# Optimization experiments

Measured on AMD Instinct MI355X. Metric: run time of the kernel, lower is better.

Reference implementation:

```python
import jax, jax.numpy as jnp
import numpy as np

B, S, H, I, E = 4, 2048, 768, 3072, 8
TOP_K = 2
ALPHA_BALANCE = 0.01
ENERGY_ALPHA = 0.0


def setup_inputs() -> dict:
    key = jax.random.key(0)
    ks = jax.random.split(key, 5)
    g = lambda k, shape: jax.random.normal(k, shape, jnp.float32) * 0.02
    return {
        "hidden_states": jax.random.normal(ks[0], (B, S, H), jnp.float32),
        "router_w": g(ks[1], (H, E)),
        "router_b": jnp.zeros((E,), jnp.float32),
        "w1": g(ks[2], (E, H, I)),
        "b1": jnp.zeros((E, I), jnp.float32),
        "w2": g(ks[3], (E, I, H)),
        "b2": jnp.zeros((E, H), jnp.float32),
    }


def reference(hidden_states, router_w, router_b, w1, b1, w2, b2):
    # --- routing: top-2 softmax gate scattered back to dense [B,S,E] ---
    router_logits = hidden_states @ router_w + router_b          # [B,S,E]
    top_v, top_i = jax.lax.top_k(router_logits, TOP_K)           # [B,S,2]
    top_w = jax.nn.softmax(top_v, axis=-1)                       # [B,S,2]
    gating = jnp.sum(
        jax.nn.one_hot(top_i, E, dtype=router_logits.dtype) * top_w[..., None],
        axis=-2,
    )                                                            # [B,S,E]

    # --- aux losses (torch .std() is unbiased, ddof=1) ---
    importance = gating.sum(axis=(0, 1))                         # [E]
    mean_imp = importance.mean()
    load_balancing_loss = ALPHA_BALANCE * (
        jnp.var(importance, ddof=1) / (mean_imp ** 2 + 1e-8)
    )
    probs_mean = gating.mean(axis=(0, 1))                        # [E]
    energy_loss = ENERGY_ALPHA * jnp.sum(probs_mean ** 2)
    aux_loss = load_balancing_loss + energy_loss

    # --- dense all-expert FFN (faithful to the naive original) ---
    # h: [B,S,E,I]; exact (erf) GELU matches torch nn.GELU default
    h = jax.nn.gelu(
        jnp.einsum("bsh,ehf->bsef", hidden_states, w1) + b1,
        approximate=False,
    )
    expert_outputs = jnp.einsum("bsef,efh->bseh", h, w2) + b2    # [B,S,E,H]
    # dropout is identity in eval mode

    # --- weighted combine (the bmm in the original) ---
    final_output = jnp.einsum("bse,bseh->bsh", gating, expert_outputs)
    return final_output, aux_loss, gating
```

## Files before the change

### kernel.cpp

```cpp
#include <hip/hip_runtime.h>
#include <math.h>

#define NB 4
#define NS 2048
#define HD 768
#define ID 3072
#define NE 8
#define NTOK (NB*NS)
#define NPAIR (NTOK*2)

#define BMF 128
#define BN1 128
#define BNF 256
#define BKF 64
#define MAXTF 136

#define BMS 32
#define KCH 128
#define NCHUNK (ID/KCH)
#define MAXTS (NPAIR/BMS + NE)
#define LDP 36

typedef unsigned short u16;
typedef __attribute__((ext_vector_type(8))) short bf16x8;
typedef __attribute__((ext_vector_type(4))) float f32x4;

__device__ __forceinline__ float bf2f(u16 u) {
  union { unsigned int i; float f; } v; v.i = ((unsigned int)u) << 16; return v.f;
}
__device__ __forceinline__ u16 f2bf(float f) {
  union { float fl; unsigned int i; } v; v.fl = f;
  unsigned int r = v.i + 0x7fffu + ((v.i >> 16) & 1u);
  return (u16)(r >> 16);
}
__device__ __forceinline__ void gload16(const void* g, void* l) {
  __builtin_amdgcn_global_load_lds(
      (const __attribute__((address_space(1))) void*)g,
      (__attribute__((address_space(3))) void*)l, 16, 0, 0);
}
__device__ __forceinline__ float gelu_fast(float x) {
  float u = 0.7978845608028654f * (x + 0.044715f * x * x * x);
  float e = __expf(2.f * u);
  float t = 1.f - 2.f / (e + 1.f);
  return 0.5f * x * (1.f + t);
}
__device__ __forceinline__ int xcd_swz_2d() {
  int nwg  = gridDim.x * gridDim.y;
  int orig = blockIdx.x + blockIdx.y * gridDim.x;
  int q = nwg >> 3, r = nwg & 7;
  int xcd = orig & 7, i = orig >> 3;
  return (xcd < r) ? (xcd * (q + 1) + i) : (r * (q + 1) + (xcd - r) * q + i);
}

__global__ __launch_bounds__(256) void router_kernel(
    const float* __restrict__ x, const float* __restrict__ rw,
    const float* __restrict__ rb, float* __restrict__ gating,
    int* __restrict__ topi, float* __restrict__ topw, u16* __restrict__ xb)
{
  int wid = threadIdx.x >> 6, lane = threadIdx.x & 63;
  int tok = blockIdx.x * 4 + wid;
  float acc[NE];
  #pragma unroll
  for (int e = 0; e < NE; ++e) acc[e] = 0.f;
  const float* xr = x + (size_t)tok * HD;
  float4 xq[3];
  #pragma unroll
  for (int r = 0; r < 3; ++r) {
    int h4 = (r*64 + lane) * 4;
    float4 xv = *(const float4*)&xr[h4];
    xq[r] = xv;
    const float4* wr = (const float4*)(rw + (size_t)h4 * NE);
    float4 a0 = wr[0], c0 = wr[1], a1 = wr[2], c1 = wr[3];
    float4 a2 = wr[4], c2 = wr[5], a3 = wr[6], c3 = wr[7];
    acc[0] += xv.x*a0.x + xv.y*a1.x + xv.z*a2.x + xv.w*a3.x;
    acc[1] += xv.x*a0.y + xv.y*a1.y + xv.z*a2.y + xv.w*a3.y;
    acc[2] += xv.x*a0.z + xv.y*a1.z + xv.z*a2.z + xv.w*a3.z;
    acc[3] += xv.x*a0.w + xv.y*a1.w + xv.z*a2.w + xv.w*a3.w;
    acc[4] += xv.x*c0.x + xv.y*c1.x + xv.z*c2.x + xv.w*c3.x;
    acc[5] += xv.x*c0.y + xv.y*c1.y + xv.z*c2.y + xv.w*c3.y;
    acc[6] += xv.x*c0.z + xv.y*c1.z + xv.z*c2.z + xv.w*c3.z;
    acc[7] += xv.x*c0.w + xv.y*c1.w + xv.z*c2.w + xv.w*c3.w;
  }
  if (xb) {
    u16* xo = xb + (size_t)tok * HD;
    #pragma unroll
    for (int r = 0; r < 3; ++r) {
      int h4 = (r*64 + lane) * 4;
      ushort4 o;
      o.x = f2bf(xq[r].x); o.y = f2bf(xq[r].y);
      o.z = f2bf(xq[r].z); o.w = f2bf(xq[r].w);
      *(ushort4*)&xo[h4] = o;
    }
  }
  #pragma unroll
  for (int off = 1; off < 64; off <<= 1) {
    #pragma unroll
    for (int e = 0; e < NE; ++e) acc[e] += __shfl_xor(acc[e], off);
  }
  float lg[NE];
  #pragma unroll
  for (int e = 0; e < NE; ++e) lg[e] = acc[e] + rb[e];
  int i0 = 0;
  #pragma unroll
  for (int e = 1; e < NE; ++e) if (lg[e] > lg[i0]) i0 = e;
  int i1 = (i0 == 0) ? 1 : 0;
  #pragma unroll
  for (int e = 0; e < NE; ++e) if (e != i0 && lg[e] > lg[i1]) i1 = e;
  float ex = expf(lg[i1] - lg[i0]);
  float s = 1.f + ex;
  float w0 = 1.f / s, w1v = ex / s;
  if (lane < NE)
    gating[(size_t)tok*NE + lane] = (lane==i0) ? w0 : (lane==i1 ? w1v : 0.f);
  if (lane == 0) {
    topi[2*tok] = i0; topi[2*tok+1] = i1;
    topw[2*tok] = w0; topw[2*tok+1] = w1v;
  }
}

__global__ __launch_bounds__(1024) void plan_kernel(
    const int* __restrict__ topi, const float* __restrict__ topw,
    int* __restrict__ offs, int* __restrict__ tilesc,
    int* __restrict__ ptok, float* __restrict__ pwv, int bm,
    float* __restrict__ aux)
{
  __shared__ int   wcnt[16][NE];
  __shared__ int   wbase[16][NE];
  __shared__ float wsum[16][NE];
  int tid = threadIdx.x, w = tid >> 6, lane = tid & 63;
  int base = w * 1024;

  int cnt[NE];
  #pragma unroll
  for (int e = 0; e < NE; ++e) cnt[e] = 0;
  #pragma unroll
  for (int it = 0; it < 16; ++it) {
    int ti = topi[base + it*64 + lane];
    #pragma unroll
    for (int e = 0; e < NE; ++e) {
      unsigned long long m = __ballot(ti == e);
      cnt[e] += __popcll(m);
    }
  }
  if (lane == 0)
    #pragma unroll
    for (int e = 0; e < NE; ++e) wcnt[w][e] = cnt[e];
  __syncthreads();

  if (tid == 0) {
    int o = 0, tt = 0;
    for (int e = 0; e < NE; ++e) {
      offs[e] = o; tilesc[e] = tt;
      int run = o, tot = 0;
      for (int ww = 0; ww < 16; ++ww) { wbase[ww][e] = run; run += wcnt[ww][e]; tot += wcnt[ww][e]; }
      o += tot;
      tt += (tot + bm - 1) / bm;
    }
    offs[NE] = o; tilesc[NE] = tt;
  }
  __syncthreads();

  int run[NE];
  float lsum[NE];
  #pragma unroll
  for (int e = 0; e < NE; ++e) { run[e] = wbase[w][e]; lsum[e] = 0.f; }
  unsigned long long lt = (1ull << lane) - 1ull;
  #pragma unroll
  for (int it = 0; it < 16; ++it) {
    int p = base + it*64 + lane;
    int ti = topi[p];
    float tw = topw[p];
    int idx = 0;
    #pragma unroll
    for (int e = 0; e < NE; ++e) {
      unsigned long long m = __ballot(ti == e);
      int r = run[e] + __popcll(m & lt);
      if (ti == e) idx = r;
      run[e] += __popcll(m);
      lsum[e] += (ti == e) ? tw : 0.f;
    }
    ptok[idx] = p >> 1;
    pwv[idx] = tw;
  }
  #pragma unroll
  for (int off = 1; off < 64; off <<= 1) {
    #pragma unroll
    for (int e = 0; e < NE; ++e) lsum[e] += __shfl_xor(lsum[e], off);
  }
  if (lane == 0)
    #pragma unroll
    for (int e = 0; e < NE; ++e) wsum[w][e] = lsum[e];
  __syncthreads();
  if (tid == 0) {
    float imp[NE];
    for (int e = 0; e < NE; ++e) {
      float s = 0.f;
      for (int ww = 0; ww < 16; ++ww) s += wsum[ww][e];
      imp[e] = s;
    }
    float mean = 0.f;
    for (int e = 0; e < NE; ++e) mean += imp[e];
    mean *= (1.f/NE);
    float var = 0.f;
    for (int e = 0; e < NE; ++e) { float d = imp[e] - mean; var += d*d; }
    var *= (1.f/(NE-1));
    aux[0] = 0.01f * var / (mean*mean + 1e-8f);
  }
}

__global__ __launch_bounds__(256) void transpose_bf16_kernel(
    const float* __restrict__ src, u16* __restrict__ dst, int R, int C)
{
  __shared__ u16 tile[64][65];
  int e = blockIdx.z;
  const float* s = src + (size_t)e * R * C;
  u16* d = dst + (size_t)e * R * C;
  int c0 = blockIdx.x * 64, r0 = blockIdx.y * 64;
  int t = threadIdx.x;
  int rr = t >> 4, c4 = (t & 15) * 4;
  #pragma unroll
  for (int rep = 0; rep < 4; ++rep) {
    int r = rr + rep * 16;
    float4 v = *(const float4*)&s[(size_t)(r0 + r) * C + c0 + c4];
    tile[r][c4+0] = f2bf(v.x); tile[r][c4+1] = f2bf(v.y);
    tile[r][c4+2] = f2bf(v.z); tile[r][c4+3] = f2bf(v.w);
  }
  __syncthreads();
  #pragma unroll
  for (int rep = 0; rep < 4; ++rep) {
    int w = t + rep * 256;
    int c = w >> 4, rq = (w & 15) * 4;
    ushort4 o;
    o.x = tile[rq+0][c]; o.y = tile[rq+1][c];
    o.z = tile[rq+2][c]; o.w = tile[rq+3][c];
    *(ushort4*)&d[(size_t)(c0 + c) * R + r0 + rq] = o;
  }
}

__global__ __launch_bounds__(256, 3) void moe_gemm1_kernel(
    const u16* __restrict__ xbf, const u16* __restrict__ w1t,
    const float* __restrict__ b1, const int* __restrict__ offs,
    const int* __restrict__ tilesc, const int* __restrict__ ptok,
    const float* __restrict__ pwv, u16* __restrict__ hbuf, int t0)
{
  __shared__ __align__(16) u16 As[BMF*BKF];
  __shared__ __align__(16) u16 Bs[BN1*BKF];
  __shared__ int   toks_s[BMF];
  __shared__ float gws_s[BMF];

  int wkid = xcd_swz_2d();
  int tile = wkid % gridDim.x;
  int n0   = (wkid / gridDim.x) * BN1;

  int t = t0 + tile;
  if (t >= tilesc[NE]) return;
  int e = 0;
  #pragma unroll
  for (int k = 1; k < NE; ++k) if (t >= tilesc[k]) e = k;
  int row0 = offs[e] + (t - tilesc[e]) * BMF;
  int nrows = offs[e+1] - row0; if (nrows > BMF) nrows = BMF;
  int tid = threadIdx.x, wid = tid >> 6, lane = tid & 63;

  if (tid < BMF) {
    int tk = -1; float g = 0.f;
    if (tid < nrows) { tk = ptok[row0 + tid]; g = pwv[row0 + tid]; }
    toks_s[tid] = tk; gws_s[tid] = g;
  }
  __syncthreads();

  int srow = tid >> 3;
  int swz  = ((tid & 7) << 4) ^ ((srow & 7) << 4);
  const char* aS[4]; const char* bS[4];
  u16* aD[4]; u16* bD[4];
  #pragma unroll
  for (int g = 0; g < 4; ++g) {
    int tk = toks_s[g*32 + srow]; if (tk < 0) tk = 0;
    aS[g] = (const char*)xbf + (size_t)tk * (HD*2) + swz;
    bS[g] = (const char*)w1t + ((size_t)e*ID + n0 + g*32 + srow) * (HD*2) + swz;
    aD[g] = As + g*2048 + wid*512;
    bD[g] = Bs + g*2048 + wid*512;
  }

  int wr = wid >> 1, wc = wid & 1;
  int lr = lane & 15, lg = lane >> 4;

  f32x4 acc[4][4];
  #pragma unroll
  for (int m = 0; m < 4; ++m)
    #pragma unroll
    for (int n = 0; n < 4; ++n) { f32x4 z = {0.f,0.f,0.f,0.f}; acc[m][n] = z; }

  for (int ks = 0; ks < HD/BKF; ++ks) {
    __syncthreads();
    int ko = ks * 128;
    #pragma unroll
    for (int g = 0; g < 4; ++g) gload16(aS[g] + ko, aD[g]);
    #pragma unroll
    for (int g = 0; g < 4; ++g) gload16(bS[g] + ko, bD[g]);
    __syncthreads();
    #pragma unroll
    for (int k2 = 0; k2 < 2; ++k2) {
      bf16x8 af[4], bfr[4];
      #pragma unroll
      for (int m = 0; m < 4; ++m) {
        int row = wr*64 + m*16 + lr;
        int bo = (k2*64 + lg*16) ^ ((row & 7) << 4);
        af[m] = *(const bf16x8*)((const char*)As + row*128 + bo);
      }
      #pragma unroll
      for (int n = 0; n < 4; ++n) {
        int row = wc*64 + n*16 + lr;
        int bo = (k2*64 + lg*16) ^ ((row & 7) << 4);
        bfr[n] = *(const bf16x8*)((const char*)Bs + row*128 + bo);
      }
      #pragma unroll
      for (int m = 0; m < 4; ++m)
        #pragma unroll
        for (int n = 0; n < 4; ++n)
          acc[m][n] = __builtin_amdgcn_mfma_f32_16x16x32_bf16(af[m], bfr[n], acc[m][n], 0, 0, 0);
    }
  }

  int rbase = wr*64, cbase = n0 + wc*64;
  const float* b1e = b1 + (size_t)e * ID;
  float b1v[4];
  #pragma unroll
  for (int n = 0; n < 4; ++n) b1v[n] = b1e[cbase + n*16 + lr];
  size_t hrow0 = (size_t)tile * BMF;
  #pragma unroll
  for (int m = 0; m < 4; ++m) {
    #pragma unroll
    for (int j = 0; j < 4; ++j) {
      int row = rbase + m*16 + lg*4 + j;
      float g = gws_s[row];
      u16* hp = hbuf + (hrow0 + row) * ID + cbase + lr;
      #pragma unroll
      for (int n = 0; n < 4; ++n) {
        float v = acc[m][n][j] + b1v[n];
        hp[n*16] = f2bf(gelu_fast(v) * g);
      }
    }
  }
}

__global__ __launch_bounds__(512, 2) void moe_gemm2_kernel(
    const u16* __restrict__ hbuf, const u16* __restrict__ w2t,
    const float* __restrict__ b2, const int* __restrict__ offs,
    const int* __restrict__ tilesc, const int* __restrict__ ptok,
    const float* __restrict__ pwv, float* __restrict__ out, int t0)
{
  __shared__ __align__(16) u16 As[BMF*BKF];
  __shared__ __align__(16) u16 Bs[BNF*BKF];
  __shared__ int   toks_s[BMF];
  __shared__ float gws_s[BMF];

  int wkid = xcd_swz_2d();
  int tile = wkid % gridDim.x;
  int n0   = (wkid / gridDim.x) * BNF;

  int t = t0 + tile;
  if (t >= tilesc[NE]) return;
  int e = 0;
  #pragma unroll
  for (int k = 1; k < NE; ++k) if (t >= tilesc[k]) e = k;
  int row0 = offs[e] + (t - tilesc[e]) * BMF;
  int nrows = offs[e+1] - row0; if (nrows > BMF) nrows = BMF;
  int tid = threadIdx.x, wid = tid >> 6, lane = tid & 63;

  if (tid < BMF) {
    int tk = -1; float g = 0.f;
    if (tid < nrows) { tk = ptok[row0 + tid]; g = pwv[row0 + tid]; }
    toks_s[tid] = tk; gws_s[tid] = g;
  }
  __syncthreads();

  int ssub = tid >> 3;
  int sbc  = (tid & 7) << 4;
  int swz  = sbc ^ ((ssub & 7) << 4);
  const char* aS0 = (const char*)hbuf + ((size_t)tile*BMF +       ssub) * (ID*2) + swz;
  const char* aS1 = (const char*)hbuf + ((size_t)tile*BMF +  64 + ssub) * (ID*2) + swz;
  const char* bS0 = (const char*)w2t + ((size_t)e*HD + n0 +       ssub) * (ID*2) + swz;
  const char* bS1 = (const char*)w2t + ((size_t)e*HD + n0 +  64 + ssub) * (ID*2) + swz;
  const char* bS2 = (const char*)w2t + ((size_t)e*HD + n0 + 128 + ssub) * (ID*2) + swz;
  const char* bS3 = (const char*)w2t + ((size_t)e*HD + n0 + 192 + ssub) * (ID*2) + swz;
  u16* aD0 = As + wid*512;
  u16* aD1 = As + 4096 + wid*512;
  u16* bD0 = Bs + wid*512;
  u16* bD1 = Bs +  4096 + wid*512;
  u16* bD2 = Bs +  8192 + wid*512;
  u16* bD3 = Bs + 12288 + wid*512;

  int wr = wid >> 2, wc = wid & 3;
  int lr = lane & 15, lg = lane >> 4;

  f32x4 acc[4][4];
  #pragma unroll
  for (int m = 0; m < 4; ++m)
    #pragma unroll
    for (int n = 0; n < 4; ++n) { f32x4 zz = {0.f,0.f,0.f,0.f}; acc[m][n] = zz; }

  for (int ks = 0; ks < ID/BKF; ++ks) {
    __syncthreads();
    int ko = ks * 128;
    gload16(aS0 + ko, aD0);
    gload16(aS1 + ko, aD1);
    gload16(bS0 + ko, bD0);
    gload16(bS1 + ko, bD1);
    gload16(bS2 + ko, bD2);
    gload16(bS3 + ko, bD3);
    __syncthreads();
    #pragma unroll
    for (int k2 = 0; k2 < 2; ++k2) {
      bf16x8 af[4], bfr[4];
      #pragma unroll
      for (int m = 0; m < 4; ++m) {
        int row = wr*64 + m*16 + lr;
        int bo = (k2*64 + lg*16) ^ ((row & 7) << 4);
        af[m] = *(const bf16x8*)((const char*)As + row*128 + bo);
      }
      #pragma unroll
      for (int n = 0; n < 4; ++n) {
        int row = wc*64 + n*16 + lr;
        int bo = (k2*64 + lg*16) ^ ((row & 7) << 4);
        bfr[n] = *(const bf16x8*)((const char*)Bs + row*128 + bo);
      }
      #pragma unroll
      for (int m = 0; m < 4; ++m)
        #pragma unroll
        for (int n = 0; n < 4; ++n)
          acc[m][n] = __builtin_amdgcn_mfma_f32_16x16x32_bf16(af[m], bfr[n], acc[m][n], 0, 0, 0);
    }
  }

  int rbase = wr*64, cbase = n0 + wc*64;
  const float* b2e = b2 + (size_t)e * HD;
  float b2v[4];
  #pragma unroll
  for (int n = 0; n < 4; ++n) b2v[n] = b2e[cbase + n*16 + lr];
  #pragma unroll
  for (int m = 0; m < 4; ++m) {
    #pragma unroll
    for (int j = 0; j < 4; ++j) {
      int row = rbase + m*16 + lg*4 + j;
      int tk = toks_s[row];
      if (tk < 0) continue;
      float g = gws_s[row];
      float* op = out + (size_t)tk * HD + cbase + lr;
      #pragma unroll
      for (int n = 0; n < 4; ++n)
        atomicAdd(&op[n*16], acc[m][n][j] + g * b2v[n]);
    }
  }
}

__global__ __launch_bounds__(512, 4) void ffn_kernel(
    const float* __restrict__ x, const float* __restrict__ w1,
    const float* __restrict__ b1, const float* __restrict__ w2,
    const float* __restrict__ b2, const int* __restrict__ offs,
    const int* __restrict__ tilesc, const int* __restrict__ ptok,
    const float* __restrict__ pwv, float* __restrict__ out)
{
  __shared__ u16 x_t[HD][LDP];
  __shared__ u16 h_t[KCH][LDP];
  __shared__ int   toks[BMS];
  __shared__ float gws[BMS];

  int bid = blockIdx.x;
  if (bid >= tilesc[NE]) return;
  int e = 0;
  #pragma unroll
  for (int k = 1; k < NE; ++k) if (bid >= tilesc[k]) e = k;
  int tile = bid - tilesc[e];
  int row0 = offs[e] + tile * BMS;
  int nrows = offs[e+1] - row0;
  if (nrows > BMS) nrows = BMS;

  int tid = threadIdx.x;
  if (tid < BMS) {
    int tk = -1; float g = 0.f;
    if (tid < nrows) { tk = ptok[row0 + tid]; g = pwv[row0 + tid]; }
    toks[tid] = tk; gws[tid] = g;
  }
  __syncthreads();

  for (int idx = tid; idx < BMS*HD; idx += 512) {
    int m = idx / HD, h = idx - m*HD;
    int tk = toks[m];
    x_t[h][m] = (tk >= 0) ? f2bf(x[(size_t)tk*HD + h]) : (u16)0;
  }

  int w4 = (tid >> 6) << 2;
  int lane = tid & 63;
  const float* w1e = w1 + (size_t)e * HD * ID;
  const float* w2e = w2 + (size_t)e * ID * HD;
  const float* b1e = b1 + (size_t)e * ID;
  const float* b2e = b2 + (size_t)e * HD;

  float acc[4][12];
  #pragma unroll
  for (int jm = 0; jm < 4; ++jm)
    #pragma unroll
    for (int jn = 0; jn < 12; ++jn) acc[jm][jn] = 0.f;

  __syncthreads();
  float gwr[4];
  #pragma unroll
  for (int jm = 0; jm < 4; ++jm) gwr[jm] = gws[w4 + jm];

  for (int c = 0; c < NCHUNK; ++c) {
    int i0 = c * KCH;
    float hb[4][2];
    #pragma unroll
    for (int jm = 0; jm < 4; ++jm) { hb[jm][0] = 0.f; hb[jm][1] = 0.f; }
    const float* p = w1e + i0 + lane;
    #pragma unroll 4
    for (int h = 0; h < HD; ++h) {
      ushort4 xu = *(const ushort4*)&x_t[h][w4];
      float wv0 = p[0];
      float wv1 = p[64];
      p += ID;
      float x0 = bf2f(xu.x), x1 = bf2f(xu.y), x2 = bf2f(xu.z), x3 = bf2f(xu.w);
      hb[0][0] += x0*wv0; hb[1][0] += x1*wv0; hb[2][0] += x2*wv0; hb[3][0] += x3*wv0;
      hb[0][1] += x0*wv1; hb[1][1] += x1*wv1; hb[2][1] += x2*wv1; hb[3][1] += x3*wv1;
    }
    float b1v0 = b1e[i0 + lane];
    float b1v1 = b1e[i0 + 64 + lane];
    __syncthreads();
    #pragma unroll
    for (int q = 0; q < 2; ++q) {
      int il = lane + 64*q;
      float bv = q ? b1v1 : b1v0;
      #pragma unroll
      for (int jm = 0; jm < 4; ++jm) {
        float v = hb[jm][q] + bv;
        v = 0.5f * v * (1.f + erff(v * 0.70710678118654752f));
        h_t[il][w4 + jm] = f2bf(v * gwr[jm]);
      }
    }
    __syncthreads();
    const float* q2 = w2e + (size_t)i0 * HD + lane;
    for (int k = 0; k < KCH; ++k) {
      ushort4 hu = *(const ushort4*)&h_t[k][w4];
      float h0 = bf2f(hu.x), h1 = bf2f(hu.y), h2 = bf2f(hu.z), h3 = bf2f(hu.w);
      #pragma unroll
      for (int jn = 0; jn < 12; ++jn) {
        float wv = q2[64*jn];
        acc[0][jn] += h0*wv; acc[1][jn] += h1*wv;
        acc[2][jn] += h2*wv; acc[3][jn] += h3*wv;
      }
      q2 += HD;
    }
  }

  #pragma unroll
  for (int jm = 0; jm < 4; ++jm) {
    int m = w4 + jm;
    int tk = toks[m];
    if (tk < 0) continue;
    float g = gwr[jm];
    float* orow = out + (size_t)tk * HD;
    #pragma unroll
    for (int jn = 0; jn < 12; ++jn) {
      int n = lane + 64*jn;
      atomicAdd(&orow[n], acc[jm][jn] + g * b2e[n]);
    }
  }
}

extern "C" void kernel_launch(void* const* d_in, const int* in_sizes, int n_in,
                              void* d_out, int out_size, void* d_ws, size_t ws_size,
                              hipStream_t stream)
{
  const float* x  = (const float*)d_in[0];
  const float* rw = (const float*)d_in[1];
  const float* rb = (const float*)d_in[2];
  const float* w1 = (const float*)d_in[3];
  const float* b1 = (const float*)d_in[4];
  const float* w2 = (const float*)d_in[5];
  const float* b2 = (const float*)d_in[6];

  float* out    = (float*)d_out;
  float* aux    = out + (size_t)NTOK * HD;
  float* gating = aux + 1;

  int*   W  = (int*)d_ws;
  float* Wf = (float*)d_ws;
  int*   offs   = W + 16;
  int*   tilesc = W + 32;
  int*   topi   = W + 64;
  float* topw   = Wf + 64 + NPAIR;
  int*   ptok   = W + 64 + 2*NPAIR;
  float* pwv    = Wf + 64 + 3*NPAIR;
  char*  wsB    = (char*)d_ws;
  const size_t OFF_XBF = 262400;
  const size_t OFF_W1T = OFF_XBF + (size_t)NTOK*HD*2;
  const size_t OFF_W2T = OFF_W1T + (size_t)NE*ID*HD*2;
  const size_t OFF_H   = OFF_W2T + (size_t)NE*ID*HD*2;
  const size_t NEED_FULL = OFF_H + (size_t)MAXTF*BMF*ID*2;

  u16* xbf = (u16*)(wsB + OFF_XBF);
  u16* w1t = (u16*)(wsB + OFF_W1T);
  u16* w2t = (u16*)(wsB + OFF_W2T);
  u16* hb  = (u16*)(wsB + OFF_H);

  bool fast = (ws_size >= NEED_FULL);

  hipMemsetAsync(d_out, 0, (size_t)NTOK * HD * sizeof(float), stream);

  router_kernel<<<NTOK/4, 256, 0, stream>>>(x, rw, rb, gating, topi, topw,
                                            fast ? xbf : (u16*)nullptr);

  if (fast) {
    plan_kernel<<<1, 1024, 0, stream>>>(topi, topw, offs, tilesc, ptok, pwv, BMF, aux);
    transpose_bf16_kernel<<<dim3(ID/64, HD/64, NE), 256, 0, stream>>>(w1, w1t, HD, ID);
    transpose_bf16_kernel<<<dim3(HD/64, ID/64, NE), 256, 0, stream>>>(w2, w2t, ID, HD);
    moe_gemm1_kernel<<<dim3(MAXTF, ID/BN1), 256, 0, stream>>>(
        xbf, w1t, b1, offs, tilesc, ptok, pwv, hb, 0);
    moe_gemm2_kernel<<<dim3(MAXTF, HD/BNF), 512, 0, stream>>>(
        hb, w2t, b2, offs, tilesc, ptok, pwv, out, 0);
  } else {
    plan_kernel<<<1, 1024, 0, stream>>>(topi, topw, offs, tilesc, ptok, pwv, BMS, aux);
    ffn_kernel<<<MAXTS, 512, 0, stream>>>(x, w1, b1, w2, b2, offs, tilesc, ptok, pwv, out);
  }
}
```

Baseline: 320.8 us.

## Fuse router and weight transposes into one prep kernel; retile gemm2 to 128x128

Router, w1 transpose and w2 transpose now run as one launch, dispatched by block index, which cuts launch overhead and lets the three jobs overlap. GEMM2 moves from 512-thread blocks with 256-wide N tiles to 256-thread blocks with 128-wide N tiles and occupancy hint 4, giving more blocks for better load balance at the cost of reloading A tiles more often. Both GEMMs switch to a 1D grid with an XCD swizzle that places the N-tiles of one M-tile next to each other, aiming for better L2 reuse of activations.

```diff
diff --git a/kernel.cpp b/kernel.cpp
--- a/kernel.cpp
+++ b/kernel.cpp
@@ -11,9 +11,11 @@
 
 #define BMF 128
 #define BN1 128
-#define BNF 256
+#define BN2 128
 #define BKF 64
 #define MAXTF 136
+#define NY1 (ID/BN1)
+#define NY2 (HD/BN2)
 
 #define BMS 32
 #define KCH 128
@@ -44,21 +46,21 @@
   float t = 1.f - 2.f / (e + 1.f);
   return 0.5f * x * (1.f + t);
 }
-__device__ __forceinline__ int xcd_swz_2d() {
-  int nwg  = gridDim.x * gridDim.y;
-  int orig = blockIdx.x + blockIdx.y * gridDim.x;
+__device__ __forceinline__ int xcd_swz_1d() {
+  int nwg  = gridDim.x;
+  int orig = blockIdx.x;
   int q = nwg >> 3, r = nwg & 7;
   int xcd = orig & 7, i = orig >> 3;
   return (xcd < r) ? (xcd * (q + 1) + i) : (r * (q + 1) + (xcd - r) * q + i);
 }
 
-__global__ __launch_bounds__(256) void router_kernel(
-    const float* __restrict__ x, const float* __restrict__ rw,
+__device__ __forceinline__ void router_body(
+    int bid, const float* __restrict__ x, const float* __restrict__ rw,
     const float* __restrict__ rb, float* __restrict__ gating,
     int* __restrict__ topi, float* __restrict__ topw, u16* __restrict__ xb)
 {
   int wid = threadIdx.x >> 6, lane = threadIdx.x & 63;
-  int tok = blockIdx.x * 4 + wid;
+  int tok = bid * 4 + wid;
   float acc[NE];
   #pragma unroll
   for (int e = 0; e < NE; ++e) acc[e] = 0.f;
@@ -117,6 +119,69 @@
   }
 }
 
+__device__ __forceinline__ void transpose_body(
+    int bx, int by, int e, const float* __restrict__ src, u16* __restrict__ dst,
+    int R, int C)
+{
+  __shared__ u16 tile[64][65];
+  const float* s = src + (size_t)e * R * C;
+  u16* d = dst + (size_t)e * R * C;
+  int c0 = bx * 64, r0 = by * 64;
+  int t = threadIdx.x;
+  int rr = t >> 4, c4 = (t & 15) * 4;
+  #pragma unroll
+  for (int rep = 0; rep < 4; ++rep) {
+    int r = rr + rep * 16;
+    float4 v = *(const float4*)&s[(size_t)(r0 + r) * C + c0 + c4];
+    tile[r][c4+0] = f2bf(v.x); tile[r][c4+1] = f2bf(v.y);
+    tile[r][c4+2] = f2bf(v.z); tile[r][c4+3] = f2bf(v.w);
+  }
+  __syncthreads();
+  #pragma unroll
+  for (int rep = 0; rep < 4; ++rep) {
+    int w = t + rep * 256;
+    int c = w >> 4, rq = (w & 15) * 4;
+    ushort4 o;
+    o.x = tile[rq+0][c]; o.y = tile[rq+1][c];
+    o.z = tile[rq+2][c]; o.w = tile[rq+3][c];
+    *(ushort4*)&d[(size_t)(c0 + c) * R + r0 + rq] = o;
+  }
+}
+
+#define NW1T ((ID/64)*(HD/64)*NE)
+#define NW2T ((HD/64)*(ID/64)*NE)
+__global__ __launch_bounds__(256) void prep_kernel(
+    const float* __restrict__ x, const float* __restrict__ rw,
+    const float* __restrict__ rb, float* __restrict__ gating,
+    int* __restrict__ topi, float* __restrict__ topw, u16* __restrict__ xb,
+    const float* __restrict__ w1, u16* __restrict__ w1t,
+    const float* __restrict__ w2, u16* __restrict__ w2t)
+{
+  int bid = blockIdx.x;
+  if (bid < NTOK/4) { router_body(bid, x, rw, rb, gating, topi, topw, xb); return; }
+  bid -= NTOK/4;
+  if (bid < NW1T) {
+    int bx = bid % (ID/64); int rest = bid / (ID/64);
+    int by = rest % (HD/64); int e = rest / (HD/64);
+    transpose_body(bx, by, e, w1, w1t, HD, ID);
+    return;
+  }
+  bid -= NW1T;
+  {
+    int bx = bid % (HD/64); int rest = bid / (HD/64);
+    int by = rest % (ID/64); int e = rest / (ID/64);
+    transpose_body(bx, by, e, w2, w2t, ID, HD);
+  }
+}
+
+__global__ __launch_bounds__(256) void router_kernel(
+    const float* __restrict__ x, const float* __restrict__ rw,
+    const float* __restrict__ rb, float* __restrict__ gating,
+    int* __restrict__ topi, float* __restrict__ topw)
+{
+  router_body(blockIdx.x, x, rw, rb, gating, topi, topw, (u16*)nullptr);
+}
+
 __global__ __launch_bounds__(1024) void plan_kernel(
     const int* __restrict__ topi, const float* __restrict__ topw,
     int* __restrict__ offs, int* __restrict__ tilesc,
@@ -207,51 +272,22 @@
   }
 }
 
-__global__ __launch_bounds__(256) void transpose_bf16_kernel(
-    const float* __restrict__ src, u16* __restrict__ dst, int R, int C)
-{
-  __shared__ u16 tile[64][65];
-  int e = blockIdx.z;
-  const float* s = src + (size_t)e * R * C;
-  u16* d = dst + (size_t)e * R * C;
-  int c0 = blockIdx.x * 64, r0 = blockIdx.y * 64;
-  int t = threadIdx.x;
-  int rr = t >> 4, c4 = (t & 15) * 4;
-  #pragma unroll
-  for (int rep = 0; rep < 4; ++rep) {
-    int r = rr + rep * 16;
-    float4 v = *(const float4*)&s[(size_t)(r0 + r) * C + c0 + c4];
-    tile[r][c4+0] = f2bf(v.x); tile[r][c4+1] = f2bf(v.y);
-    tile[r][c4+2] = f2bf(v.z); tile[r][c4+3] = f2bf(v.w);
-  }
-  __syncthreads();
-  #pragma unroll
-  for (int rep = 0; rep < 4; ++rep) {
-    int w = t + rep * 256;
-    int c = w >> 4, rq = (w & 15) * 4;
-    ushort4 o;
-    o.x = tile[rq+0][c]; o.y = tile[rq+1][c];
-    o.z = tile[rq+2][c]; o.w = tile[rq+3][c];
-    *(ushort4*)&d[(size_t)(c0 + c) * R + r0 + rq] = o;
-  }
-}
-
 __global__ __launch_bounds__(256, 3) void moe_gemm1_kernel(
     const u16* __restrict__ xbf, const u16* __restrict__ w1t,
     const float* __restrict__ b1, const int* __restrict__ offs,
     const int* __restrict__ tilesc, const int* __restrict__ ptok,
-    const float* __restrict__ pwv, u16* __restrict__ hbuf, int t0)
+    const float* __restrict__ pwv, u16* __restrict__ hbuf)
 {
   __shared__ __align__(16) u16 As[BMF*BKF];
   __shared__ __align__(16) u16 Bs[BN1*BKF];
   __shared__ int   toks_s[BMF];
   __shared__ float gws_s[BMF];
 
-  int wkid = xcd_swz_2d();
-  int tile = wkid % gridDim.x;
-  int n0   = (wkid / gridDim.x) * BN1;
-
-  int t = t0 + tile;
+  int wkid = xcd_swz_1d();
+  int tile = wkid / NY1;
+  int n0   = (wkid % NY1) * BN1;
+
+  int t = tile;
   if (t >= tilesc[NE]) return;
   int e = 0;
   #pragma unroll
@@ -342,22 +378,22 @@
   }
 }
 
-__global__ __launch_bounds__(512, 2) void moe_gemm2_kernel(
+__global__ __launch_bounds__(256, 4) void moe_gemm2_kernel(
     const u16* __restrict__ hbuf, const u16* __restrict__ w2t,
     const float* __restrict__ b2, const int* __restrict__ offs,
     const int* __restrict__ tilesc, const int* __restrict__ ptok,
-    const float* __restrict__ pwv, float* __restrict__ out, int t0)
+    const float* __restrict__ pwv, float* __restrict__ out)
 {
   __shared__ __align__(16) u16 As[BMF*BKF];
-  __shared__ __align__(16) u16 Bs[BNF*BKF];
+  __shared__ __align__(16) u16 Bs[BN2*BKF];
   __shared__ int   toks_s[BMF];
   __shared__ float gws_s[BMF];
 
-  int wkid = xcd_swz_2d();
-  int tile = wkid % gridDim.x;
-  int n0   = (wkid / gridDim.x) * BNF;
-
-  int t = t0 + tile;
+  int wkid = xcd_swz_1d();
+  int tile = wkid / NY2;
+  int n0   = (wkid % NY2) * BN2;
+
+  int t = tile;
   if (t >= tilesc[NE]) return;
   int e = 0;
   #pragma unroll
@@ -373,40 +409,34 @@
   }
   __syncthreads();
 
-  int ssub = tid >> 3;
-  int sbc  = (tid & 7) << 4;
-  int swz  = sbc ^ ((ssub & 7) << 4);
-  const char* aS0 = (const char*)hbuf + ((size_t)tile*BMF +       ssub) * (ID*2) + swz;
-  const char* aS1 = (const char*)hbuf + ((size_t)tile*BMF +  64 + ssub) * (ID*2) + swz;
-  const char* bS0 = (const char*)w2t + ((size_t)e*HD + n0 +       ssub) * (ID*2) + swz;
-  const char* bS1 = (const char*)w2t + ((size_t)e*HD + n0 +  64 + ssub) * (ID*2) + swz;
-  const char* bS2 = (const char*)w2t + ((size_t)e*HD + n0 + 128 + ssub) * (ID*2) + swz;
-  const char* bS3 = (const char*)w2t + ((size_t)e*HD + n0 + 192 + ssub) * (ID*2) + swz;
-  u16* aD0 = As + wid*512;
-  u16* aD1 = As + 4096 + wid*512;
-  u16* bD0 = Bs + wid*512;
-  u16* bD1 = Bs +  4096 + wid*512;
-  u16* bD2 = Bs +  8192 + wid*512;
-  u16* bD3 = Bs + 12288 + wid*512;
-
-  int wr = wid >> 2, wc = wid & 3;
+  int srow = tid >> 3;
+  int swz  = ((tid & 7) << 4) ^ ((srow & 7) << 4);
+  const char* aS[4]; const char* bS[4];
+  u16* aD[4]; u16* bD[4];
+  #pragma unroll
+  for (int g = 0; g < 4; ++g) {
+    aS[g] = (const char*)hbuf + ((size_t)tile*BMF + g*32 + srow) * (ID*2) + swz;
+    bS[g] = (const char*)w2t + ((size_t)e*HD + n0 + g*32 + srow) * (ID*2) + swz;
+    aD[g] = As + g*2048 + wid*512;
+    bD[g] = Bs + g*2048 + wid*512;
+  }
+
+  int wr = wid >> 1, wc = wid & 1;
   int lr = lane & 15, lg = lane >> 4;
 
   f32x4 acc[4][4];
   #pragma unroll
   for (int m = 0; m < 4; ++m)
     #pragma unroll
-    for (int n = 0; n < 4; ++n) { f32x4 zz = {0.f,0.f,0.f,0.f}; acc[m][n] = zz; }
+    for (int n = 0; n < 4; ++n) { f32x4 z = {0.f,0.f,0.f,0.f}; acc[m][n] = z; }
 
   for (int ks = 0; ks < ID/BKF; ++ks) {
     __syncthreads();
     int ko = ks * 128;
-    gload16(aS0 + ko, aD0);
-    gload16(aS1 + ko, aD1);
-    gload16(bS0 + ko, bD0);
-    gload16(bS1 + ko, bD1);
-    gload16(bS2 + ko, bD2);
-    gload16(bS3 + ko, bD3);
+    #pragma unroll
+    for (int g = 0; g < 4; ++g) gload16(aS[g] + ko, aD[g]);
+    #pragma unroll
+    for (int g = 0; g < 4; ++g) gload16(bS[g] + ko, bD[g]);
     __syncthreads();
     #pragma unroll
     for (int k2 = 0; k2 < 2; ++k2) {
@@ -606,18 +636,16 @@
 
   hipMemsetAsync(d_out, 0, (size_t)NTOK * HD * sizeof(float), stream);
 
-  router_kernel<<<NTOK/4, 256, 0, stream>>>(x, rw, rb, gating, topi, topw,
-                                            fast ? xbf : (u16*)nullptr);
-
   if (fast) {
+    prep_kernel<<<NTOK/4 + NW1T + NW2T, 256, 0, stream>>>(
+        x, rw, rb, gating, topi, topw, xbf, w1, w1t, w2, w2t);
     plan_kernel<<<1, 1024, 0, stream>>>(topi, topw, offs, tilesc, ptok, pwv, BMF, aux);
-    transpose_bf16_kernel<<<dim3(ID/64, HD/64, NE), 256, 0, stream>>>(w1, w1t, HD, ID);
-    transpose_bf16_kernel<<<dim3(HD/64, ID/64, NE), 256, 0, stream>>>(w2, w2t, ID, HD);
-    moe_gemm1_kernel<<<dim3(MAXTF, ID/BN1), 256, 0, stream>>>(
-        xbf, w1t, b1, offs, tilesc, ptok, pwv, hb, 0);
-    moe_gemm2_kernel<<<dim3(MAXTF, HD/BNF), 512, 0, stream>>>(
-        hb, w2t, b2, offs, tilesc, ptok, pwv, out, 0);
+    moe_gemm1_kernel<<<MAXTF * NY1, 256, 0, stream>>>(
+        xbf, w1t, b1, offs, tilesc, ptok, pwv, hb);
+    moe_gemm2_kernel<<<MAXTF * NY2, 256, 0, stream>>>(
+        hb, w2t, b2, offs, tilesc, ptok, pwv, out);
   } else {
+    router_kernel<<<NTOK/4, 256, 0, stream>>>(x, rw, rb, gating, topi, topw);
     plan_kernel<<<1, 1024, 0, stream>>>(topi, topw, offs, tilesc, ptok, pwv, BMS, aux);
     ffn_kernel<<<MAXTS, 512, 0, stream>>>(x, w1, b1, w2, b2, offs, tilesc, ptok, pwv, out);
   }
```

Result: faster. 303.1 us, median of 2 (-5.5%).
